# Performance work log

Measured on AMD Instinct MI355X. Metric: run time of the kernel, lower is better.

The kernel has to match this reference:

```python
import jax, jax.numpy as jnp
import numpy as np

B, T, D, E, TOP_K = 8, 2048, 512, 8, 2


def setup_inputs() -> dict:
    key = jax.random.key(0)
    ks = jax.random.split(key, 8)
    s = 0.02
    return {
        "x": jax.random.normal(ks[0], (B, T, D), dtype=jnp.float32),
        "eps": jax.random.normal(ks[1], (B, T, E), dtype=jnp.float32),
        "Wr": jax.random.normal(ks[2], (D, E), dtype=jnp.float32) * s,
        "br": jnp.zeros((E,), dtype=jnp.float32),
        "Wn": jax.random.normal(ks[3], (D, E), dtype=jnp.float32) * s,
        "bn": jnp.zeros((E,), dtype=jnp.float32),
        "Wk": jax.random.normal(ks[4], (E, D, D), dtype=jnp.float32) * s,
        "bk": jnp.zeros((E, D), dtype=jnp.float32),
    }


def reference(x, eps, Wr, br, Wn, bn, Wk, bk):
    # Noisy top-k router (NoisyTopkRouter.forward)
    logits = jnp.einsum("btd,de->bte", x, Wr) + br            # [B,T,E]
    noise_logits = jnp.einsum("btd,de->bte", x, Wn) + bn      # [B,T,E]
    noisy = logits + eps * jax.nn.softplus(noise_logits)      # [B,T,E]
    _, top_idx = jax.lax.top_k(noisy, TOP_K)                  # [B,T,k]
    # mask[b,t,e] = True iff expert e is in the token's top-k
    topk_mask = jax.nn.one_hot(top_idx, E, dtype=jnp.float32).sum(-2) > 0
    sparse_logits = jnp.where(topk_mask, noisy, -jnp.inf)
    gating = jax.nn.softmax(sparse_logits, axis=-1)           # zero for non-top-k experts
    # Dense dispatch: every expert's Linear applied to all tokens, then
    # gating (zero outside top-k) selects/scales — same math as the masked
    # gather + per-expert Linear + gating scale in SparseMoE.forward.
    expert_out = jnp.einsum("btd,edh->bteh", x, Wk) + bk      # [B,T,E,D]
    out = jnp.einsum("bte,bteh->bth", gating, expert_out)     # [B,T,D]
    return out
```

## Files before the change

### kernel.cpp

```cpp
#include <hip/hip_runtime.h>
#include <hip/hip_bf16.h>
#include <math.h>

#define B_    8
#define T_    2048
#define NTOK  (B_ * T_)
#define D_    512
#define E_    8
#define NPAIR 28
#define CAP   NTOK

#define RV_TOK    16
#define RV_THR    256
#define XS_STRIDE 132
#define WS_FLOATS 2108

typedef __attribute__((ext_vector_type(4))) float f32x4;
typedef __attribute__((ext_vector_type(8))) short short8;

__device__ __forceinline__ void async_load16(const void* g, void* l) {
    __builtin_amdgcn_global_load_lds(
        (const __attribute__((address_space(1))) unsigned int*)g,
        (__attribute__((address_space(3))) unsigned int*)l,
        16, 0, 0);
}

__global__ __launch_bounds__(256) void transpose_wk(
    const float* __restrict__ Wk, __hip_bfloat16* __restrict__ Wkt)
{
    __shared__ float tile[32][33];
    const int e  = blockIdx.z;
    const int d0 = blockIdx.x * 32;
    const int h0 = blockIdx.y * 32;
    const int tx = threadIdx.x, ty = threadIdx.y;

    const float* src = Wk + ((size_t)e * D_ + d0) * D_ + h0;
    #pragma unroll
    for (int r = ty; r < 32; r += 8)
        tile[r][tx] = src[(size_t)r * D_ + tx];
    __syncthreads();
    __hip_bfloat16* dst = Wkt + ((size_t)e * D_ + h0) * D_ + d0;
    #pragma unroll
    for (int r = ty; r < 32; r += 8)
        dst[(size_t)r * D_ + tx] = __float2bfloat16(tile[tx][r]);
}

__global__ __launch_bounds__(RV_THR) void router_kernel(
    const float* __restrict__ x,
    const float* __restrict__ eps,
    const float* __restrict__ Wr,
    const float* __restrict__ br,
    const float* __restrict__ Wn,
    const float* __restrict__ bn,
    __hip_bfloat16* __restrict__ xb,
    uint4* __restrict__ top2)
{
    __shared__ float xs[RV_TOK * XS_STRIDE];
    __shared__ float wsh[WS_FLOATS];

    const int tid  = threadIdx.x;
    const int tok0 = blockIdx.x * RV_TOK;
    const int lane = tid & 63, wv = tid >> 6;
    const int kidx = lane >> 2, ts = lane & 3;
    const int tl = wv * 4 + ts;
    const int wk = tid >> 1, wh = tid & 1;

    float acc[16];
    #pragma unroll
    for (int c = 0; c < 16; ++c) acc[c] = 0.f;

    for (int kc = 0; kc < D_; kc += 128) {
        #pragma unroll
        for (int it = 0; it < 2; ++it) {
            const int f   = it * RV_THR + tid;
            const int row = f >> 5, col = (f & 31) * 4;
            const f32x4 v = *(const f32x4*)(x + (size_t)(tok0 + row) * D_ + kc + col);
            *(f32x4*)(xs + row * XS_STRIDE + col) = v;
            union { __hip_bfloat16 h[4]; uint2 u; } cv;
            cv.h[0] = __float2bfloat16(v.x); cv.h[1] = __float2bfloat16(v.y);
            cv.h[2] = __float2bfloat16(v.z); cv.h[3] = __float2bfloat16(v.w);
            *(uint2*)(xb + (size_t)(tok0 + row) * D_ + kc + col) = cv.u;
        }
        {
            const float* src = (wh ? Wn : Wr) + (size_t)(kc + wk) * E_;
            const f32x4 w0 = *(const f32x4*)(src);
            const f32x4 w1 = *(const f32x4*)(src + 4);
            float* dst = wsh + wk * 16 + (wk >> 3) * 4 + wh * 8;
            *(f32x4*)(dst)     = w0;
            *(f32x4*)(dst + 4) = w1;
        }
        __syncthreads();

        const float* xra = xs + tl * XS_STRIDE + kidx * 8;
        const f32x4 xa0 = *(const f32x4*)(xra);
        const f32x4 xa1 = *(const f32x4*)(xra + 4);
        const float* wbase = wsh + kidx * 132;
        #pragma unroll
        for (int kk = 0; kk < 8; ++kk) {
            const float xav = (kk < 4) ? xa0[kk] : xa1[kk - 4];
            const float* wrow = wbase + kk * 16;
            #pragma unroll
            for (int c4 = 0; c4 < 4; ++c4) {
                const f32x4 w = *(const f32x4*)(wrow + c4 * 4);
                #pragma unroll
                for (int c = 0; c < 4; ++c)
                    acc[c4 * 4 + c] = fmaf(xav, w[c], acc[c4 * 4 + c]);
            }
        }
        __syncthreads();
    }

    #pragma unroll
    for (int off = 4; off < 64; off <<= 1) {
        #pragma unroll
        for (int c = 0; c < 16; ++c)
            acc[c] += __shfl_xor(acc[c], off);
    }

    if (lane < 4) {
        const int tok = tok0 + tl;
        float nv[8];
        #pragma unroll
        for (int e = 0; e < 8; ++e) {
            const float nl = acc[8 + e] + bn[e];
            const float sp = fmaxf(nl, 0.f) + log1pf(expf(-fabsf(nl)));
            nv[e] = acc[e] + br[e] + eps[(size_t)tok * E_ + e] * sp;
        }
        int i1 = 0; float v1 = nv[0];
        #pragma unroll
        for (int e = 1; e < 8; ++e)
            if (nv[e] > v1) { v1 = nv[e]; i1 = e; }
        int i2 = -1; float v2 = -3.4e38f;
        #pragma unroll
        for (int e = 0; e < 8; ++e)
            if (e != i1 && nv[e] > v2) { v2 = nv[e]; i2 = e; }
        const float t  = expf(v2 - v1);
        const float g1 = 1.f / (1.f + t);
        const float g2 = t / (1.f + t);
        top2[tok] = make_uint4((unsigned)i1 | ((unsigned)i2 << 8),
                               __float_as_uint(g1), __float_as_uint(g2), 0u);
    }
}

__global__ __launch_bounds__(256) void bucket_kernel(
    const uint4* __restrict__ top2,
    int* __restrict__ counts,
    uint4* __restrict__ entries)
{
    __shared__ int hist[NPAIR];
    __shared__ int base[NPAIR];
    const int tid = threadIdx.x;
    const int tok = blockIdx.x * 256 + tid;
    if (tid < NPAIR) hist[tid] = 0;
    __syncthreads();
    const uint4 t = top2[tok];
    const int i1 = t.x & 0xff, i2 = (t.x >> 8) & 0xff;
    const int a = min(i1, i2), b = max(i1, i2);
    const unsigned ga = (i1 < i2) ? t.y : t.z;
    const unsigned gb = (i1 < i2) ? t.z : t.y;
    const int p = a * (15 - a) / 2 + (b - a - 1);
    const int l = atomicAdd(&hist[p], 1);
    __syncthreads();
    if (tid < NPAIR) base[tid] = atomicAdd(counts + tid, hist[tid]);
    __syncthreads();
    entries[(size_t)p * CAP + base[p] + l] = make_uint4((unsigned)tok, ga, gb, 0u);
}

__global__ __launch_bounds__(256, 2) void moe_gemm(
    const __hip_bfloat16* __restrict__ xb,
    const __hip_bfloat16* __restrict__ wkt,
    const float* __restrict__ bk,
    const int* __restrict__ counts,
    const uint4* __restrict__ entries,
    float* __restrict__ out)
{
    constexpr int BM = 128, BN = 128, BK = 32;
    __shared__ __hip_bfloat16 As[BM * BK];
    __shared__ __hip_bfloat16 Bs[2][BN * BK];
    __shared__ uint4 ent[BM];

    const int p  = blockIdx.z;
    const int mt = blockIdx.y;
    const int nt = blockIdx.x;
    const int cnt = counts[p];
    if (mt * BM >= cnt) return;

    int e1 = 0, rem = p;
    while (rem >= 7 - e1) { rem -= 7 - e1; ++e1; }
    const int e2 = e1 + 1 + rem;

    const int tid = threadIdx.x;
    const int wave = tid >> 6, lane = tid & 63;

    if (tid < BM) {
        const int idx = mt * BM + tid;
        ent[tid] = (idx < cnt) ? entries[(size_t)p * CAP + idx]
                               : make_uint4(0u, 0u, 0u, 0u);
    }
    __syncthreads();

    const int quad = lane >> 4, lr = lane & 15;
    const int wm = wave >> 1, wn = wave & 1;
    const int sub = lane >> 2, part = lane & 3;

    f32x4 accA[4][4], accB[4][4];
    #pragma unroll
    for (int i = 0; i < 4; ++i)
        #pragma unroll
        for (int j = 0; j < 4; ++j) {
            accA[i][j] = (f32x4){0.f, 0.f, 0.f, 0.f};
            accB[i][j] = (f32x4){0.f, 0.f, 0.f, 0.f};
        }

    const size_t tok0 = ent[wave * 32 + sub].x;
    const size_t tok1 = ent[wave * 32 + 16 + sub].x;
    const size_t brow1 = (size_t)e1 * D_ + nt * BN + wave * 32 + sub;
    const size_t brow2 = (size_t)e2 * D_ + nt * BN + wave * 32 + sub;

    for (int k0 = 0; k0 < D_; k0 += BK) {
        async_load16(xb + tok0 * D_ + k0 + part * 8, As + (wave * 32) * BK);
        async_load16(xb + tok1 * D_ + k0 + part * 8, As + (wave * 32 + 16) * BK);
        async_load16(wkt + brow1 * D_ + k0 + part * 8, Bs[0] + (wave * 32) * BK);
        async_load16(wkt + (brow1 + 16) * D_ + k0 + part * 8, Bs[0] + (wave * 32 + 16) * BK);
        async_load16(wkt + brow2 * D_ + k0 + part * 8, Bs[1] + (wave * 32) * BK);
        async_load16(wkt + (brow2 + 16) * D_ + k0 + part * 8, Bs[1] + (wave * 32 + 16) * BK);
        __syncthreads();

        short8 a[4], b1[4], b2[4];
        #pragma unroll
        for (int i = 0; i < 4; ++i)
            a[i] = *(const short8*)(As + (wm * 64 + i * 16 + lr) * BK + quad * 8);
        #pragma unroll
        for (int j = 0; j < 4; ++j) {
            b1[j] = *(const short8*)(Bs[0] + (wn * 64 + j * 16 + lr) * BK + quad * 8);
            b2[j] = *(const short8*)(Bs[1] + (wn * 64 + j * 16 + lr) * BK + quad * 8);
        }
        #pragma unroll
        for (int i = 0; i < 4; ++i)
            #pragma unroll
            for (int j = 0; j < 4; ++j) {
                accA[i][j] = __builtin_amdgcn_mfma_f32_16x16x32_bf16(a[i], b1[j], accA[i][j], 0, 0, 0);
                accB[i][j] = __builtin_amdgcn_mfma_f32_16x16x32_bf16(a[i], b2[j], accB[i][j], 0, 0, 0);
            }
        __syncthreads();
    }

    const int colbase = nt * BN + wn * 64 + lr;
    float bkA[4], bkB[4];
    #pragma unroll
    for (int j = 0; j < 4; ++j) {
        bkA[j] = bk[e1 * D_ + colbase + j * 16];
        bkB[j] = bk[e2 * D_ + colbase + j * 16];
    }

    #pragma unroll
    for (int i = 0; i < 4; ++i) {
        #pragma unroll
        for (int r = 0; r < 4; ++r) {
            const int row = wm * 64 + i * 16 + quad * 4 + r;
            if (mt * BM + row < cnt) {
                const uint4 en = ent[row];
                const float ga = __uint_as_float(en.y);
                const float gb = __uint_as_float(en.z);
                float* orow = out + (size_t)en.x * D_ + colbase;
                #pragma unroll
                for (int j = 0; j < 4; ++j)
                    orow[j * 16] = ga * (accA[i][j][r] + bkA[j])
                                 + gb * (accB[i][j][r] + bkB[j]);
            }
        }
    }
}

extern "C" void kernel_launch(void* const* d_in, const int* in_sizes, int n_in,
                              void* d_out, int out_size, void* d_ws, size_t ws_size,
                              hipStream_t stream) {
    const float* x   = (const float*)d_in[0];
    const float* eps = (const float*)d_in[1];
    const float* Wr  = (const float*)d_in[2];
    const float* br  = (const float*)d_in[3];
    const float* Wn  = (const float*)d_in[4];
    const float* bn  = (const float*)d_in[5];
    const float* Wk  = (const float*)d_in[6];
    const float* bk  = (const float*)d_in[7];
    float* out = (float*)d_out;

    char* ws = (char*)d_ws;
    size_t off = 0;
    int* counts = (int*)(ws + off);                     off += 256;
    uint4* entries = (uint4*)(ws + off);                off += (size_t)NPAIR * CAP * 16;
    __hip_bfloat16* xb = (__hip_bfloat16*)(ws + off);   off += (size_t)NTOK * D_ * 2;
    __hip_bfloat16* wkt = (__hip_bfloat16*)(ws + off);  off += (size_t)E_ * D_ * D_ * 2;
    uint4* top2 = (uint4*)(ws + off);                   off += (size_t)NTOK * 16;
    (void)ws_size;

    hipMemsetAsync(counts, 0, NPAIR * sizeof(int), stream);

    transpose_wk<<<dim3(16, 16, E_), dim3(32, 8), 0, stream>>>(Wk, wkt);
    router_kernel<<<dim3(NTOK / RV_TOK), dim3(RV_THR), 0, stream>>>(
        x, eps, Wr, br, Wn, bn, xb, top2);
    bucket_kernel<<<dim3(NTOK / 256), dim3(256), 0, stream>>>(top2, counts, entries);
    moe_gemm<<<dim3(D_ / 128, CAP / 128, NPAIR), dim3(256), 0, stream>>>(
        xb, wkt, bk, counts, entries, out);
}
```

Baseline: 168.9 us.

## Compact MoE GEMM grid via worklist, double-buffer LDS, restructure tile layout

```diff
diff --git a/kernel.cpp b/kernel.cpp
--- a/kernel.cpp
+++ b/kernel.cpp
@@ -9,6 +9,8 @@
 #define E_    8
 #define NPAIR 28
 #define CAP   NTOK
+
+#define WL_MAX 160
 
 #define RV_TOK    16
 #define RV_THR    256
@@ -166,24 +168,46 @@
     entries[(size_t)p * CAP + base[p] + l] = make_uint4((unsigned)tok, ga, gb, 0u);
 }
 
+__global__ __launch_bounds__(64) void build_wl(
+    const int* __restrict__ counts, int* __restrict__ wl)
+{
+    const int t = threadIdx.x;
+    const int nm = (t < NPAIR) ? ((counts[t] + 127) >> 7) : 0;
+    int inc = nm;
+    #pragma unroll
+    for (int d = 1; d < 64; d <<= 1) {
+        const int v = __shfl_up(inc, d);
+        if (t >= d) inc += v;
+    }
+    if (t == 63) wl[0] = inc;
+    const int ex = inc - nm;
+    for (int m = 0; m < nm; ++m)
+        wl[1 + ex + m] = (t << 8) | m;
+}
+
 __global__ __launch_bounds__(256, 2) void moe_gemm(
     const __hip_bfloat16* __restrict__ xb,
     const __hip_bfloat16* __restrict__ wkt,
     const float* __restrict__ bk,
     const int* __restrict__ counts,
     const uint4* __restrict__ entries,
+    const int* __restrict__ wl,
     float* __restrict__ out)
 {
     constexpr int BM = 128, BN = 128, BK = 32;
-    __shared__ __hip_bfloat16 As[BM * BK];
-    __shared__ __hip_bfloat16 Bs[2][BN * BK];
+    __shared__ __hip_bfloat16 As[2][BM * BK];
+    __shared__ __hip_bfloat16 Bs[2][2][BN * BK];
     __shared__ uint4 ent[BM];
 
-    const int p  = blockIdx.z;
-    const int mt = blockIdx.y;
-    const int nt = blockIdx.x;
+    const int id = blockIdx.x;
+    const int g = id >> 5, r = id & 31;
+    const int nt = r >> 3;
+    const int mi = g * 8 + (r & 7);
+    const int nmtot = wl[0];
+    if (mi >= nmtot) return;
+    const int we = wl[1 + mi];
+    const int p = we >> 8, mt = we & 255;
     const int cnt = counts[p];
-    if (mt * BM >= cnt) return;
 
     int e1 = 0, rem = p;
     while (rem >= 7 - e1) { rem -= 7 - e1; ++e1; }
@@ -201,7 +225,13 @@
 
     const int quad = lane >> 4, lr = lane & 15;
     const int wm = wave >> 1, wn = wave & 1;
-    const int sub = lane >> 2, part = lane & 3;
+
+    const size_t tokLo = ent[lane].x;
+    const size_t tokHi = ent[64 + lane].x;
+    const __hip_bfloat16* gA0 = xb + tokLo * D_ + wave * 8;
+    const __hip_bfloat16* gA1 = xb + tokHi * D_ + wave * 8;
+    const __hip_bfloat16* gB1 = wkt + ((size_t)(e1 * D_ + nt * BN) + lane) * D_ + wave * 8;
+    const __hip_bfloat16* gB2 = wkt + ((size_t)(e2 * D_ + nt * BN) + lane) * D_ + wave * 8;
 
     f32x4 accA[4][4], accB[4][4];
     #pragma unroll
@@ -212,38 +242,56 @@
             accB[i][j] = (f32x4){0.f, 0.f, 0.f, 0.f};
         }
 
-    const size_t tok0 = ent[wave * 32 + sub].x;
-    const size_t tok1 = ent[wave * 32 + 16 + sub].x;
-    const size_t brow1 = (size_t)e1 * D_ + nt * BN + wave * 32 + sub;
-    const size_t brow2 = (size_t)e2 * D_ + nt * BN + wave * 32 + sub;
-
-    for (int k0 = 0; k0 < D_; k0 += BK) {
-        async_load16(xb + tok0 * D_ + k0 + part * 8, As + (wave * 32) * BK);
-        async_load16(xb + tok1 * D_ + k0 + part * 8, As + (wave * 32 + 16) * BK);
-        async_load16(wkt + brow1 * D_ + k0 + part * 8, Bs[0] + (wave * 32) * BK);
-        async_load16(wkt + (brow1 + 16) * D_ + k0 + part * 8, Bs[0] + (wave * 32 + 16) * BK);
-        async_load16(wkt + brow2 * D_ + k0 + part * 8, Bs[1] + (wave * 32) * BK);
-        async_load16(wkt + (brow2 + 16) * D_ + k0 + part * 8, Bs[1] + (wave * 32 + 16) * BK);
+#define STAGE(buf, k0) do {                                        \
+        __hip_bfloat16* aB  = &As[buf][wave * 1024];               \
+        __hip_bfloat16* b1B = &Bs[buf][0][wave * 1024];            \
+        __hip_bfloat16* b2B = &Bs[buf][1][wave * 1024];            \
+        async_load16(gA0 + (k0), aB);                              \
+        async_load16(gA1 + (k0), aB + 512);                        \
+        async_load16(gB1 + (k0), b1B);                             \
+        async_load16(gB1 + 64 * D_ + (k0), b1B + 512);             \
+        async_load16(gB2 + (k0), b2B);                             \
+        async_load16(gB2 + 64 * D_ + (k0), b2B + 512);             \
+    } while (0)
+
+#define COMPUTE(buf) do {                                                      \
+        const __hip_bfloat16* aP  = &As[buf][quad * 1024 + lr * 8];            \
+        const __hip_bfloat16* b1P = &Bs[buf][0][quad * 1024 + lr * 8];         \
+        const __hip_bfloat16* b2P = &Bs[buf][1][quad * 1024 + lr * 8];         \
+        short8 a[4], b1[4], b2[4];                                             \
+        _Pragma("unroll")                                                      \
+        for (int i = 0; i < 4; ++i)                                            \
+            a[i] = *(const short8*)(aP + (wm * 64 + i * 16) * 8);              \
+        _Pragma("unroll")                                                      \
+        for (int j = 0; j < 4; ++j) {                                          \
+            b1[j] = *(const short8*)(b1P + (wn * 64 + j * 16) * 8);            \
+            b2[j] = *(const short8*)(b2P + (wn * 64 + j * 16) * 8);            \
+        }                                                                      \
+        _Pragma("unroll")                                                      \
+        for (int i = 0; i < 4; ++i)                                            \
+            _Pragma("unroll")                                                  \
+            for (int j = 0; j < 4; ++j) {                                      \
+                accA[i][j] = __builtin_amdgcn_mfma_f32_16x16x32_bf16(          \
+                    a[i], b1[j], accA[i][j], 0, 0, 0);                         \
+                accB[i][j] = __builtin_amdgcn_mfma_f32_16x16x32_bf16(          \
+                    a[i], b2[j], accB[i][j], 0, 0, 0);                         \
+            }                                                                  \
+    } while (0)
+
+    STAGE(0, 0);
+    __syncthreads();
+
+    int cur = 0;
+    for (int k0 = BK; k0 < D_; k0 += BK) {
+        STAGE(cur ^ 1, k0);
+        COMPUTE(cur);
         __syncthreads();
-
-        short8 a[4], b1[4], b2[4];
-        #pragma unroll
-        for (int i = 0; i < 4; ++i)
-            a[i] = *(const short8*)(As + (wm * 64 + i * 16 + lr) * BK + quad * 8);
-        #pragma unroll
-        for (int j = 0; j < 4; ++j) {
-            b1[j] = *(const short8*)(Bs[0] + (wn * 64 + j * 16 + lr) * BK + quad * 8);
-            b2[j] = *(const short8*)(Bs[1] + (wn * 64 + j * 16 + lr) * BK + quad * 8);
-        }
-        #pragma unroll
-        for (int i = 0; i < 4; ++i)
-            #pragma unroll
-            for (int j = 0; j < 4; ++j) {
-                accA[i][j] = __builtin_amdgcn_mfma_f32_16x16x32_bf16(a[i], b1[j], accA[i][j], 0, 0, 0);
-                accB[i][j] = __builtin_amdgcn_mfma_f32_16x16x32_bf16(a[i], b2[j], accB[i][j], 0, 0, 0);
-            }
-        __syncthreads();
-    }
+        cur ^= 1;
+    }
+    COMPUTE(cur);
+
+#undef STAGE
+#undef COMPUTE
 
     const int colbase = nt * BN + wn * 64 + lr;
     float bkA[4], bkB[4];
@@ -256,8 +304,8 @@
     #pragma unroll
     for (int i = 0; i < 4; ++i) {
         #pragma unroll
-        for (int r = 0; r < 4; ++r) {
-            const int row = wm * 64 + i * 16 + quad * 4 + r;
+        for (int rr = 0; rr < 4; ++rr) {
+            const int row = wm * 64 + i * 16 + quad * 4 + rr;
             if (mt * BM + row < cnt) {
                 const uint4 en = ent[row];
                 const float ga = __uint_as_float(en.y);
@@ -265,8 +313,8 @@
                 float* orow = out + (size_t)en.x * D_ + colbase;
                 #pragma unroll
                 for (int j = 0; j < 4; ++j)
-                    orow[j * 16] = ga * (accA[i][j][r] + bkA[j])
-                                 + gb * (accB[i][j][r] + bkB[j]);
+                    orow[j * 16] = ga * (accA[i][j][rr] + bkA[j])
+                                 + gb * (accB[i][j][rr] + bkB[j]);
             }
         }
     }
@@ -292,6 +340,7 @@
     __hip_bfloat16* xb = (__hip_bfloat16*)(ws + off);   off += (size_t)NTOK * D_ * 2;
     __hip_bfloat16* wkt = (__hip_bfloat16*)(ws + off);  off += (size_t)E_ * D_ * D_ * 2;
     uint4* top2 = (uint4*)(ws + off);                   off += (size_t)NTOK * 16;
+    int* wl = (int*)(ws + off);                         off += 1024;
     (void)ws_size;
 
     hipMemsetAsync(counts, 0, NPAIR * sizeof(int), stream);
@@ -300,6 +349,7 @@
     router_kernel<<<dim3(NTOK / RV_TOK), dim3(RV_THR), 0, stream>>>(
         x, eps, Wr, br, Wn, bn, xb, top2);
     bucket_kernel<<<dim3(NTOK / 256), dim3(256), 0, stream>>>(top2, counts, entries);
-    moe_gemm<<<dim3(D_ / 128, CAP / 128, NPAIR), dim3(256), 0, stream>>>(
-        xb, wkt, bk, counts, entries, out);
-}
+    build_wl<<<dim3(1), dim3(64), 0, stream>>>(counts, wl);
+    moe_gemm<<<dim3(WL_MAX * 4), dim3(256), 0, stream>>>(
+        xb, wkt, bk, counts, entries, wl, out);
+}
```

New measurement: 188.0 us. +11.3%, slower.
